# Kernel tuning notes

Measured on AMD Instinct MI355X. Metric: run time of the kernel, lower is better.

## Reference

```python
import jax, jax.numpy as jnp
import numpy as np

D = 256    # lstm_encoder_size
B = 1024   # batch (number of agents/trajectories)
T = 512    # prediction horizon (recurrence steps)
EPS = 1e-5


def setup_inputs() -> dict:
    key = jax.random.key(0)
    k = jax.random.split(key, 10)
    s = 1.0 / np.sqrt(D)
    return {
        "KS_ALL": jax.random.normal(k[0], (1, B, D), jnp.float32),
        "next_vf": jax.random.normal(k[1], (B, T), jnp.float32),
        # Koopman operators (torch Linear stores [out, in]; no bias)
        "A_w": jax.random.normal(k[2], (D, D), jnp.float32) * (0.4 * s),  # contractive
        "B_w": jax.random.normal(k[3], (D, 1), jnp.float32) * s,
        # decoder params (liner_dec=False)
        "W0": jax.random.normal(k[4], (2 * D, D), jnp.float32) * s,
        "b0": jnp.zeros((2 * D,), jnp.float32),
        "W1": jax.random.normal(k[5], (D, 2 * D), jnp.float32) / np.sqrt(2.0 * D),
        "b1": jnp.zeros((D,), jnp.float32),
        "ln_g": jnp.ones((D,), jnp.float32),
        "ln_b": jnp.zeros((D,), jnp.float32),
        "W2": jax.random.normal(k[6], (D, D), jnp.float32) * s,
        "b2": jnp.zeros((D,), jnp.float32),
        "W3": jax.random.normal(k[7], (3, D), jnp.float32) * s,
        "b3": jnp.zeros((3,), jnp.float32),
    }


def _layer_norm(x, g, b):
    mu = jnp.mean(x, axis=-1, keepdims=True)
    var = jnp.var(x, axis=-1, keepdims=True)
    return (x - mu) * jax.lax.rsqrt(var + EPS) * g + b


def reference(KS_ALL, next_vf, A_w, B_w, W0, b0, W1, b1, ln_g, ln_b, W2, b2, W3, b3):
    # train_flag=True -> use only the first time slice of KS_ALL
    ks0 = KS_ALL[0]                 # [B, D]
    u = next_vf.T                   # [T, B] time-major, matches permute(1,0,2)
    b_vec = B_w[:, 0]               # [D]  (Linear(1, D) on scalar input)

    def step(ks, u_t):
        ks_new = ks @ A_w.T + u_t[:, None] * b_vec[None, :]  # [B, D]
        return ks_new, ks_new

    _, ks_seq = jax.lax.scan(step, ks0, u)                   # [T, B, D]
    KS_pre = jnp.concatenate([ks0[None], ks_seq], axis=0)    # [T+1, B, D]

    # nonlinear decoder (eval mode: dropout is identity; use_elu=True)
    s1 = jnp.tanh(KS_pre @ W0.T + b0)          # [T+1, B, 2D]
    s2 = jnp.tanh(s1 @ W1.T + b1)              # [T+1, B, D]
    s2 = _layer_norm(KS_pre + s2, ln_g, ln_b)  # AddAndNorm
    s3 = jax.nn.elu(s2 @ W2.T + b2)
    OS = s3 @ W3.T + b3                        # [T+1, B, 3]
    return KS_pre, OS
```

## Files before the change

### kernel.cpp

```cpp
#include <hip/hip_runtime.h>

typedef unsigned short u16;
typedef __attribute__((ext_vector_type(8))) short bf16x8;
typedef __attribute__((ext_vector_type(4))) short bf16x4;
typedef __attribute__((ext_vector_type(4))) float f32x4;

#define MFMA16(a, b, c) __builtin_amdgcn_mfma_f32_16x16x32_bf16((a), (b), (c), 0, 0, 0)

#define OFF_UPAD 0
#define OFF_KS0  589824
#define OFF_W0   851968
#define OFF_W1   983040
#define OFF_W2   1114112
#define OFF_CRT  1179648
#define OFF_P    1196032
#define OFF_H1   5455872
#define OFF_S2   73089024
#define WS_END_U16 106905600ULL
#define OS_OFF   134479872

__device__ __forceinline__ u16 f2bf(float f) {
  union { float f; unsigned int i; } v; v.f = f;
  return (u16)((v.i + 0x7fffu + ((v.i >> 16) & 1u)) >> 16);
}
__device__ __forceinline__ float bf2f(u16 u) {
  union { unsigned int i; float f; } v; v.i = ((unsigned int)u) << 16;
  return v.f;
}
__device__ __forceinline__ float fast_tanh(float x) {
  float e = __expf(2.0f * x);
  return 1.0f - __fdividef(2.0f, e + 1.0f);
}

__global__ void k_prep(const float* __restrict__ KS_ALL, const float* __restrict__ next_vf,
                       const float* __restrict__ A_w, const float* __restrict__ W0,
                       const float* __restrict__ W1, const float* __restrict__ W2,
                       u16* __restrict__ ws) {
  int idx = blockIdx.x * 256 + threadIdx.x;
  if (idx < 589824) {
    int r = idx / 576, c = idx % 576;
    ws[OFF_UPAD + idx] = (c < 64) ? (u16)0 : f2bf(next_vf[r * 512 + c - 64]);
    return;
  }
  idx -= 589824;
  if (idx < 262144) { ws[OFF_KS0 + idx] = f2bf(KS_ALL[idx]); return; }
  idx -= 262144;
  if (idx < 131072) { ws[OFF_W0 + idx] = f2bf(W0[idx]); return; }
  idx -= 131072;
  if (idx < 131072) { ws[OFF_W1 + idx] = f2bf(W1[idx]); return; }
  idx -= 131072;
  if (idx < 65536)  { ws[OFF_W2 + idx] = f2bf(W2[idx]); return; }
  idx -= 65536;
  if (idx < 65536) {
    int r = idx >> 8, c = idx & 255;
    ws[OFF_P + idx] = (r == c) ? (u16)0x3F80 : (u16)0;
    ws[OFF_P + 65536 + idx] = f2bf(A_w[idx]);
  }
}

__global__ __launch_bounds__(512) void k_pow(u16* __restrict__ ws, int s) {
  const u16* P = ws + OFF_P;
  int j = blockIdx.y + 1;
  int mh = blockIdx.x;
  int lane = threadIdx.x & 63, w = threadIdx.x >> 6;
  int wm = w >> 2, wn = w & 3;
  int lg = lane >> 4, ll = lane & 15;
  const u16* Am = P + s * 65536;
  const u16* Bm = P + j * 65536;
  f32x4 acc[4][4];
  f32x4 z = {0.f, 0.f, 0.f, 0.f};
#pragma unroll
  for (int mi = 0; mi < 4; ++mi)
#pragma unroll
    for (int ni = 0; ni < 4; ++ni) acc[mi][ni] = z;
#pragma unroll
  for (int ks = 0; ks < 8; ++ks) {
    bf16x8 a[4], b[4];
    int kk = ks * 32 + lg * 8;
#pragma unroll
    for (int mi = 0; mi < 4; ++mi) {
      int row = mh * 128 + wm * 64 + mi * 16 + ll;
      a[mi] = *(const bf16x8*)(Am + row * 256 + kk);
    }
#pragma unroll
    for (int ni = 0; ni < 4; ++ni) {
      int col = wn * 64 + ni * 16 + ll;
#pragma unroll
      for (int e = 0; e < 8; ++e) b[ni][e] = (short)Bm[(kk + e) * 256 + col];
    }
#pragma unroll
    for (int mi = 0; mi < 4; ++mi)
#pragma unroll
      for (int ni = 0; ni < 4; ++ni) acc[mi][ni] = MFMA16(a[mi], b[ni], acc[mi][ni]);
  }
  u16* Pd = ws + OFF_P + (s + j) * 65536;
#pragma unroll
  for (int mi = 0; mi < 4; ++mi)
#pragma unroll
    for (int ni = 0; ni < 4; ++ni)
#pragma unroll
      for (int r = 0; r < 4; ++r) {
        int row = mh * 128 + wm * 64 + mi * 16 + lg * 4 + r;
        int col = wn * 64 + ni * 16 + ll;
        Pd[row * 256 + col] = f2bf(acc[mi][ni][r]);
      }
}

__global__ void k_crevt(const float* __restrict__ B_w, u16* __restrict__ ws) {
  int s = blockIdx.x;
  int n = threadIdx.x;
  const u16* Pr = ws + OFF_P + (63 - s) * 65536 + n * 256;
  float acc = 0.f;
  for (int k = 0; k < 256; ++k) acc += bf2f(Pr[k]) * B_w[k];
  ws[OFF_CRT + n * 64 + s] = f2bf(acc);
}


__global__ __launch_bounds__(512) void k_ks(const u16* __restrict__ ws, float* __restrict__ out) {
  __shared__ __align__(16) float Hf[32 * 260];
  const int t  = blockIdx.y;
  const int R0 = blockIdx.x * 64;
  const int tid = threadIdx.x;
  const int lane = tid & 63, w = tid >> 6;
  const int lg = lane >> 4, ll = lane & 15;
  f32x4 z = {0.f, 0.f, 0.f, 0.f};

  f32x4 acc[4][2];
#pragma unroll
  for (int mi = 0; mi < 4; ++mi)
#pragma unroll
    for (int ni = 0; ni < 2; ++ni) acc[mi][ni] = z;
  {
    const u16* CrevT = ws + OFF_CRT;
#pragma unroll
    for (int ksu = 0; ksu < 2; ++ksu) {
      bf16x8 au[4];
#pragma unroll
      for (int mi = 0; mi < 4; ++mi) {
        const u16* up = ws + OFF_UPAD + (R0 + mi * 16 + ll) * 576 + t + ksu * 32 + lg * 8;
#pragma unroll
        for (int e = 0; e < 8; ++e) au[mi][e] = (short)up[e];
      }
#pragma unroll
      for (int ni = 0; ni < 2; ++ni) {
        int n = w * 32 + ni * 16 + ll;
        bf16x8 bfr = *(const bf16x8*)(CrevT + n * 64 + ksu * 32 + lg * 8);
#pragma unroll
        for (int mi = 0; mi < 4; ++mi) acc[mi][ni] = MFMA16(au[mi], bfr, acc[mi][ni]);
      }
    }
    if (t < 64) {
      const u16* Pt = ws + OFF_P + t * 65536;
      const u16* ks0b = ws + OFF_KS0;
#pragma unroll
      for (int ks = 0; ks < 8; ++ks) {
        bf16x8 a[4], b[2];
#pragma unroll
        for (int mi = 0; mi < 4; ++mi)
          a[mi] = *(const bf16x8*)(ks0b + (R0 + mi * 16 + ll) * 256 + ks * 32 + lg * 8);
#pragma unroll
        for (int ni = 0; ni < 2; ++ni)
          b[ni] = *(const bf16x8*)(Pt + (w * 32 + ni * 16 + ll) * 256 + ks * 32 + lg * 8);
#pragma unroll
        for (int mi = 0; mi < 4; ++mi)
#pragma unroll
          for (int ni = 0; ni < 2; ++ni) acc[mi][ni] = MFMA16(a[mi], b[ni], acc[mi][ni]);
      }
    }
  }
#pragma unroll 1
  for (int p = 0; p < 2; ++p) {
#pragma unroll
    for (int mi2 = 0; mi2 < 2; ++mi2) {
      int mi = p * 2 + mi2;
#pragma unroll
      for (int ni = 0; ni < 2; ++ni)
#pragma unroll
        for (int r = 0; r < 4; ++r)
          Hf[(mi2 * 16 + lg * 4 + r) * 260 + w * 32 + ni * 16 + ll] = acc[mi][ni][r];
    }
    __syncthreads();
    float* ob = out + (size_t)t * 262144 + (size_t)(R0 + p * 32) * 256;
#pragma unroll
    for (int it = 0; it < 4; ++it) {
      int idx = it * 512 + tid;
      int row = idx >> 6, c4 = idx & 63;
      f32x4 v = *(const f32x4*)(Hf + row * 260 + c4 * 4);
      *(f32x4*)(ob + row * 256 + c4 * 4) = v;
    }
    __syncthreads();
  }
}

__global__ __launch_bounds__(512) void k_l1(const u16* __restrict__ ws,
                                            const float* __restrict__ outf,
                                            const float* __restrict__ b0,
                                            u16* __restrict__ h1, int t0) {
  __shared__ __align__(16) u16 Xb[16896];
  __shared__ __align__(16) u16 Hb[16896];
  __shared__ float pb0s[512];
  const int by = blockIdx.y;
  const int t  = t0 + by;
  const int R0 = blockIdx.x * 64;
  const int tid = threadIdx.x;
  const int lane = tid & 63, w = tid >> 6;
  const int lg = lane >> 4, ll = lane & 15;
  f32x4 z = {0.f, 0.f, 0.f, 0.f};

  pb0s[tid] = b0[tid];
  {
    const float* xs = outf + (size_t)t * 262144 + (size_t)R0 * 256;
#pragma unroll
    for (int it = 0; it < 8; ++it) {
      int idx = it * 512 + tid;
      int row = idx >> 6, c4 = idx & 63;
      f32x4 v = *(const f32x4*)(xs + row * 256 + c4 * 4);
      bf16x4 h;
#pragma unroll
      for (int e = 0; e < 4; ++e) h[e] = (short)f2bf(v[e]);
      int byt = (((row << 9) + ((c4 >> 1) << 4)) ^ ((row & 7) << 4)) + ((c4 & 1) << 3);
      *(bf16x4*)(Xb + (byt >> 1)) = h;
    }
  }
  __syncthreads();

  const u16* W0b = ws + OFF_W0;
#pragma unroll 1
  for (int nh = 0; nh < 2; ++nh) {
    f32x4 acc[4][2];
#pragma unroll
    for (int mi = 0; mi < 4; ++mi)
#pragma unroll
      for (int ni = 0; ni < 2; ++ni) acc[mi][ni] = z;
#pragma unroll
    for (int ks = 0; ks < 8; ++ks) {
      bf16x8 b[2];
#pragma unroll
      for (int ni = 0; ni < 2; ++ni) {
        int n = nh * 256 + w * 32 + ni * 16 + ll;
        b[ni] = *(const bf16x8*)(W0b + n * 256 + ks * 32 + lg * 8);
      }
#pragma unroll
      for (int mi = 0; mi < 4; ++mi) {
        int rl = mi * 16 + ll;
        int byt = ((rl << 9) + ks * 64 + (lg << 4)) ^ ((rl & 7) << 4);
        bf16x8 a = *(const bf16x8*)(Xb + (byt >> 1));
#pragma unroll
        for (int ni = 0; ni < 2; ++ni) acc[mi][ni] = MFMA16(a, b[ni], acc[mi][ni]);
      }
    }
#pragma unroll
    for (int mi = 0; mi < 4; ++mi)
#pragma unroll
      for (int ni = 0; ni < 2; ++ni)
#pragma unroll
        for (int r = 0; r < 4; ++r) {
          int rl = mi * 16 + lg * 4 + r;
          int col = w * 32 + ni * 16 + ll;
          Hb[rl * 264 + col] = f2bf(fast_tanh(acc[mi][ni][r] + pb0s[nh * 256 + col]));
        }
    __syncthreads();
    u16* hd = h1 + ((size_t)(by * 1024 + R0)) * 512 + nh * 256;
#pragma unroll
    for (int it = 0; it < 4; ++it) {
      int idx = it * 512 + tid;
      int row = idx >> 5, cq = idx & 31;
      bf16x8 v = *(const bf16x8*)(Hb + row * 264 + cq * 8);
      *(bf16x8*)(hd + row * 512 + cq * 8) = v;
    }
    __syncthreads();
  }
}

__global__ __launch_bounds__(512) void k_l2(const u16* __restrict__ ws,
                                            const float* __restrict__ outf,
                                            const float* __restrict__ b1,
                                            const float* __restrict__ lng,
                                            const float* __restrict__ lnb,
                                            const u16* __restrict__ h1,
                                            u16* __restrict__ s2, int t0) {
  __shared__ __align__(16) u16 Hs[16896];
  __shared__ __align__(16) u16 Rb[16896];
  __shared__ float par[768];
  float* pb1 = par;
  float* pg  = par + 256;
  float* pbt = par + 512;
  const int by = blockIdx.y;
  const int t  = t0 + by;
  const int R0 = blockIdx.x * 64;
  const int tid = threadIdx.x;
  const int lane = tid & 63, w = tid >> 6;
  const int lg = lane >> 4, ll = lane & 15;
  f32x4 z = {0.f, 0.f, 0.f, 0.f};

  if (tid < 256) { pb1[tid] = b1[tid]; pg[tid] = lng[tid]; pbt[tid] = lnb[tid]; }

  f32x4 accL2[4][2];
#pragma unroll
  for (int mi = 0; mi < 4; ++mi)
#pragma unroll
    for (int ni = 0; ni < 2; ++ni) accL2[mi][ni] = z;

  const u16* W1b = ws + OFF_W1;
  const u16* h1b = h1 + ((size_t)(by * 1024 + R0)) * 512;
#pragma unroll 1
  for (int kh = 0; kh < 2; ++kh) {
#pragma unroll
    for (int it = 0; it < 4; ++it) {
      int idx = it * 512 + tid;
      int row = idx >> 5, cq = idx & 31;
      bf16x8 v = *(const bf16x8*)(h1b + row * 512 + kh * 256 + cq * 8);
      int byt = ((row << 9) + (cq << 4)) ^ ((row & 7) << 4);
      *(bf16x8*)(Hs + (byt >> 1)) = v;
    }
    __syncthreads();
#pragma unroll
    for (int ks = 0; ks < 8; ++ks) {
      bf16x8 b[2];
#pragma unroll
      for (int ni = 0; ni < 2; ++ni) {
        int n = w * 32 + ni * 16 + ll;
        b[ni] = *(const bf16x8*)(W1b + n * 512 + kh * 256 + ks * 32 + lg * 8);
      }
#pragma unroll
      for (int mi = 0; mi < 4; ++mi) {
        int rl = mi * 16 + ll;
        int byt = ((rl << 9) + ks * 64 + (lg << 4)) ^ ((rl & 7) << 4);
        bf16x8 a = *(const bf16x8*)(Hs + (byt >> 1));
#pragma unroll
        for (int ni = 0; ni < 2; ++ni) accL2[mi][ni] = MFMA16(a, b[ni], accL2[mi][ni]);
      }
    }
    __syncthreads();
  }

  {
    const float* xs = outf + (size_t)t * 262144 + (size_t)R0 * 256;
#pragma unroll
    for (int mi = 0; mi < 4; ++mi)
#pragma unroll
      for (int ni = 0; ni < 2; ++ni)
#pragma unroll
        for (int r = 0; r < 4; ++r) {
          int rl = mi * 16 + lg * 4 + r;
          int col = w * 32 + ni * 16 + ll;
          float v = xs[rl * 256 + col] + fast_tanh(accL2[mi][ni][r] + pb1[col]);
          Rb[rl * 264 + col] = f2bf(v);
        }
  }
  __syncthreads();

  {
    int row = tid >> 3, jq = tid & 7;
    u16* hr = Rb + row * 264 + jq * 32;
    bf16x8 chv[4];
#pragma unroll
    for (int q = 0; q < 4; ++q) chv[q] = *(const bf16x8*)(hr + q * 8);
    float s = 0.f, ss = 0.f;
#pragma unroll
    for (int q = 0; q < 4; ++q)
#pragma unroll
      for (int e = 0; e < 8; ++e) { float v = bf2f((u16)chv[q][e]); s += v; ss += v * v; }
    s += __shfl_xor(s, 1);  s += __shfl_xor(s, 2);  s += __shfl_xor(s, 4);
    ss += __shfl_xor(ss, 1); ss += __shfl_xor(ss, 2); ss += __shfl_xor(ss, 4);
    float mu = s * 0.00390625f;
    float var = ss * 0.00390625f - mu * mu;
    float rstd = rsqrtf(var + 1e-5f);
#pragma unroll
    for (int q = 0; q < 4; ++q) {
      bf16x8 o;
#pragma unroll
      for (int e = 0; e < 8; ++e) {
        int col = jq * 32 + q * 8 + e;
        float v = (bf2f((u16)chv[q][e]) - mu) * rstd * pg[col] + pbt[col];
        o[e] = (short)f2bf(v);
      }
      *(bf16x8*)(hr + q * 8) = o;
    }
  }
  __syncthreads();

  {
    u16* sd = s2 + ((size_t)(by * 1024 + R0)) * 256;
#pragma unroll
    for (int it = 0; it < 4; ++it) {
      int idx = it * 512 + tid;
      int row = idx >> 5, cq = idx & 31;
      bf16x8 v = *(const bf16x8*)(Rb + row * 264 + cq * 8);
      *(bf16x8*)(sd + row * 256 + cq * 8) = v;
    }
  }
}

__global__ __launch_bounds__(512) void k_l3(const u16* __restrict__ ws,
                                            const float* __restrict__ b2,
                                            const float* __restrict__ W3,
                                            const float* __restrict__ b3,
                                            const u16* __restrict__ s2,
                                            float* __restrict__ out, int t0) {
  __shared__ __align__(16) u16 Sb[16896];
  __shared__ __align__(16) u16 Eb[16896];
  __shared__ float par[1028];
  float* pb2 = par;
  float* pW3 = par + 256;
  float* pb3 = par + 1024;
  const int by = blockIdx.y;
  const int t  = t0 + by;
  const int R0 = blockIdx.x * 64;
  const int tid = threadIdx.x;
  const int lane = tid & 63, w = tid >> 6;
  const int lg = lane >> 4, ll = lane & 15;
  f32x4 z = {0.f, 0.f, 0.f, 0.f};

  if (tid < 256) pb2[tid] = b2[tid];
  if (tid < 512) pW3[tid] = W3[tid];
  if (tid < 256) pW3[512 + tid] = W3[512 + tid];
  if (tid < 4) pb3[tid] = (tid < 3) ? b3[tid] : 0.f;

  {
    const u16* sb = s2 + ((size_t)(by * 1024 + R0)) * 256;
#pragma unroll
    for (int it = 0; it < 4; ++it) {
      int idx = it * 512 + tid;
      int row = idx >> 5, cq = idx & 31;
      bf16x8 v = *(const bf16x8*)(sb + row * 256 + cq * 8);
      int byt = ((row << 9) + (cq << 4)) ^ ((row & 7) << 4);
      *(bf16x8*)(Sb + (byt >> 1)) = v;
    }
  }
  __syncthreads();

  f32x4 acc[4][2];
#pragma unroll
  for (int mi = 0; mi < 4; ++mi)
#pragma unroll
    for (int ni = 0; ni < 2; ++ni) acc[mi][ni] = z;
  {
    const u16* W2b = ws + OFF_W2;
#pragma unroll
    for (int ks = 0; ks < 8; ++ks) {
      bf16x8 b[2];
#pragma unroll
      for (int ni = 0; ni < 2; ++ni) {
        int n = w * 32 + ni * 16 + ll;
        b[ni] = *(const bf16x8*)(W2b + n * 256 + ks * 32 + lg * 8);
      }
#pragma unroll
      for (int mi = 0; mi < 4; ++mi) {
        int rl = mi * 16 + ll;
        int byt = ((rl << 9) + ks * 64 + (lg << 4)) ^ ((rl & 7) << 4);
        bf16x8 a = *(const bf16x8*)(Sb + (byt >> 1));
#pragma unroll
        for (int ni = 0; ni < 2; ++ni) acc[mi][ni] = MFMA16(a, b[ni], acc[mi][ni]);
      }
    }
  }
#pragma unroll
  for (int mi = 0; mi < 4; ++mi)
#pragma unroll
    for (int ni = 0; ni < 2; ++ni)
#pragma unroll
      for (int r = 0; r < 4; ++r) {
        int rl = mi * 16 + lg * 4 + r;
        int col = w * 32 + ni * 16 + ll;
        float v = acc[mi][ni][r] + pb2[col];
        v = v > 0.f ? v : (__expf(v) - 1.f);
        Eb[rl * 264 + col] = f2bf(v);
      }
  __syncthreads();

  {
    int row = tid >> 3, jq = tid & 7;
    const u16* xr = Eb + row * 264 + jq * 32;
    float d0 = 0.f, d1 = 0.f, d2 = 0.f;
#pragma unroll
    for (int q = 0; q < 4; ++q) {
      bf16x8 c = *(const bf16x8*)(xr + q * 8);
#pragma unroll
      for (int e = 0; e < 8; ++e) {
        float v = bf2f((u16)c[e]);
        int col = jq * 32 + q * 8 + e;
        d0 += v * pW3[col]; d1 += v * pW3[256 + col]; d2 += v * pW3[512 + col];
      }
    }
    d0 += __shfl_xor(d0, 1); d0 += __shfl_xor(d0, 2); d0 += __shfl_xor(d0, 4);
    d1 += __shfl_xor(d1, 1); d1 += __shfl_xor(d1, 2); d1 += __shfl_xor(d1, 4);
    d2 += __shfl_xor(d2, 1); d2 += __shfl_xor(d2, 2); d2 += __shfl_xor(d2, 4);
    if (jq == 0) {
      int grow = R0 + row;
      int ob = OS_OFF + t * 3072 + grow * 3;
      out[ob]     = d0 + pb3[0];
      out[ob + 1] = d1 + pb3[1];
      out[ob + 2] = d2 + pb3[2];
    }
  }
}

__global__ __launch_bounds__(512) void k_fused(
    const u16* __restrict__ ws,
    const float* __restrict__ b0, const float* __restrict__ b1,
    const float* __restrict__ lng, const float* __restrict__ lnb,
    const float* __restrict__ b2, const float* __restrict__ W3,
    const float* __restrict__ b3, float* __restrict__ out) {
  __shared__ __align__(16) u16 Xb[16896];
  __shared__ __align__(16) unsigned char Hraw[33792];
  __shared__ float par[2308];
  u16* Hb = (u16*)Hraw;
  float* Hf = (float*)Hraw;
  float* pb0 = par;
  float* pb1 = par + 512;
  float* pg  = par + 768;
  float* pbt = par + 1024;
  float* pb2 = par + 1280;
  float* pW3 = par + 1536;
  float* pb3 = par + 2304;
  const int t  = blockIdx.y;
  const int R0 = blockIdx.x * 64;
  const int tid = threadIdx.x;
  const int lane = tid & 63, w = tid >> 6;
  const int lg = lane >> 4, ll = lane & 15;
  pb0[tid] = b0[tid];
  if (tid < 256) { pb1[tid] = b1[tid]; pg[tid] = lng[tid]; pbt[tid] = lnb[tid]; pb2[tid] = b2[tid]; }
  if (tid < 512) pW3[tid] = W3[tid];
  if (tid < 256) pW3[512 + tid] = W3[512 + tid];
  if (tid < 4) pb3[tid] = (tid < 3) ? b3[tid] : 0.f;
  f32x4 z = {0.f, 0.f, 0.f, 0.f};
  f32x4 acc[4][2];
#pragma unroll
  for (int mi = 0; mi < 4; ++mi)
#pragma unroll
    for (int ni = 0; ni < 2; ++ni) acc[mi][ni] = z;
  {
    const u16* CrevT = ws + OFF_CRT;
#pragma unroll
    for (int ksu = 0; ksu < 2; ++ksu) {
      bf16x8 au[4];
#pragma unroll
      for (int mi = 0; mi < 4; ++mi) {
        const u16* up = ws + OFF_UPAD + (R0 + mi * 16 + ll) * 576 + t + ksu * 32 + lg * 8;
#pragma unroll
        for (int e = 0; e < 8; ++e) au[mi][e] = (short)up[e];
      }
#pragma unroll
      for (int ni = 0; ni < 2; ++ni) {
        int n = w * 32 + ni * 16 + ll;
        bf16x8 bfr = *(const bf16x8*)(CrevT + n * 64 + ksu * 32 + lg * 8);
#pragma unroll
        for (int mi = 0; mi < 4; ++mi) acc[mi][ni] = MFMA16(au[mi], bfr, acc[mi][ni]);
      }
    }
    if (t < 64) {
      const u16* Pt = ws + OFF_P + t * 65536;
      const u16* ks0b = ws + OFF_KS0;
#pragma unroll
      for (int ks = 0; ks < 8; ++ks) {
        bf16x8 a[4], b[2];
#pragma unroll
        for (int mi = 0; mi < 4; ++mi)
          a[mi] = *(const bf16x8*)(ks0b + (R0 + mi * 16 + ll) * 256 + ks * 32 + lg * 8);
#pragma unroll
        for (int ni = 0; ni < 2; ++ni)
          b[ni] = *(const bf16x8*)(Pt + (w * 32 + ni * 16 + ll) * 256 + ks * 32 + lg * 8);
#pragma unroll
        for (int mi = 0; mi < 4; ++mi)
#pragma unroll
          for (int ni = 0; ni < 2; ++ni) acc[mi][ni] = MFMA16(a[mi], b[ni], acc[mi][ni]);
      }
    }
  }
#pragma unroll 1
  for (int p = 0; p < 2; ++p) {
#pragma unroll
    for (int mi2 = 0; mi2 < 2; ++mi2) {
      int mi = p * 2 + mi2;
#pragma unroll
      for (int ni = 0; ni < 2; ++ni)
#pragma unroll
        for (int r = 0; r < 4; ++r)
          Hf[(mi2 * 16 + lg * 4 + r) * 260 + w * 32 + ni * 16 + ll] = acc[mi][ni][r];
    }
    __syncthreads();
    float* ob = out + (size_t)t * 262144 + (size_t)(R0 + p * 32) * 256;
#pragma unroll
    for (int it = 0; it < 4; ++it) {
      int idx = it * 512 + tid;
      int row = idx >> 6, c4 = idx & 63;
      f32x4 v = *(const f32x4*)(Hf + row * 260 + c4 * 4);
      *(f32x4*)(ob + row * 256 + c4 * 4) = v;
      int rl = p * 32 + row;
      bf16x4 h;
#pragma unroll
      for (int e = 0; e < 4; ++e) h[e] = (short)f2bf(v[e]);
      int byt = (((rl << 9) + ((c4 >> 1) << 4)) ^ ((rl & 7) << 4)) + ((c4 & 1) << 3);
      *(bf16x4*)(Xb + (byt >> 1)) = h;
    }
    __syncthreads();
  }
  const u16* W0b = ws + OFF_W0;
  const u16* W1b = ws + OFF_W1;
  f32x4 accL2[4][2];
#pragma unroll
  for (int mi = 0; mi < 4; ++mi)
#pragma unroll
    for (int ni = 0; ni < 2; ++ni) accL2[mi][ni] = z;
  const int colL1 = w * 16 + ll;
#pragma unroll 1
  for (int q = 0; q < 4; ++q) {
    f32x4 accQ[4];
#pragma unroll
    for (int mi = 0; mi < 4; ++mi) accQ[mi] = z;
#pragma unroll
    for (int ks = 0; ks < 8; ++ks) {
      bf16x8 b = *(const bf16x8*)(W0b + (q * 128 + colL1) * 256 + ks * 32 + lg * 8);
#pragma unroll
      for (int mi = 0; mi < 4; ++mi) {
        int rl = mi * 16 + ll;
        int byt = ((rl << 9) + ks * 64 + (lg << 4)) ^ ((rl & 7) << 4);
        bf16x8 a = *(const bf16x8*)(Xb + (byt >> 1));
        accQ[mi] = MFMA16(a, b, accQ[mi]);
      }
    }
#pragma unroll
    for (int mi = 0; mi < 4; ++mi)
#pragma unroll
      for (int r = 0; r < 4; ++r) {
        int rl2 = mi * 16 + lg * 4 + r;
        float v = fast_tanh(accQ[mi][r] + pb0[q * 128 + colL1]);
        int byt = ((rl2 << 8) + (colL1 << 1)) ^ ((rl2 & 7) << 4);
        Hb[byt >> 1] = f2bf(v);
      }
    __syncthreads();
#pragma unroll
    for (int ks2 = 0; ks2 < 4; ++ks2) {
      bf16x8 bf0 = *(const bf16x8*)(W1b + (w * 32 + ll) * 512 + q * 128 + ks2 * 32 + lg * 8);
      bf16x8 bf1 = *(const bf16x8*)(W1b + (w * 32 + 16 + ll) * 512 + q * 128 + ks2 * 32 + lg * 8);
#pragma unroll
      for (int mi = 0; mi < 4; ++mi) {
        int rl = mi * 16 + ll;
        int byt = ((rl << 8) + ks2 * 64 + (lg << 4)) ^ ((rl & 7) << 4);
        bf16x8 a = *(const bf16x8*)(Hb + (byt >> 1));
        accL2[mi][0] = MFMA16(a, bf0, accL2[mi][0]);
        accL2[mi][1] = MFMA16(a, bf1, accL2[mi][1]);
      }
    }
    __syncthreads();
  }
#pragma unroll
  for (int mi = 0; mi < 4; ++mi)
#pragma unroll
    for (int ni = 0; ni < 2; ++ni)
#pragma unroll
      for (int r = 0; r < 4; ++r) {
        int rl = mi * 16 + lg * 4 + r;
        int col = w * 32 + ni * 16 + ll;
        float v = fast_tanh(accL2[mi][ni][r] + pb1[col]);
        int bx = ((rl << 9) + (col << 1)) ^ ((rl & 7) << 4);
        v += bf2f(Xb[bx >> 1]);
        Hb[rl * 264 + col] = f2bf(v);
      }
  __syncthreads();
  {
    int row = tid >> 3, jq = tid & 7;
    u16* hr = Hb + row * 264 + jq * 32;
    bf16x8 chv[4];
#pragma unroll
    for (int q = 0; q < 4; ++q) chv[q] = *(const bf16x8*)(hr + q * 8);
    float s = 0.f, ss = 0.f;
#pragma unroll
    for (int q = 0; q < 4; ++q)
#pragma unroll
      for (int e = 0; e < 8; ++e) { float v = bf2f((u16)chv[q][e]); s += v; ss += v * v; }
    s += __shfl_xor(s, 1);  s += __shfl_xor(s, 2);  s += __shfl_xor(s, 4);
    ss += __shfl_xor(ss, 1); ss += __shfl_xor(ss, 2); ss += __shfl_xor(ss, 4);
    float mu = s * 0.00390625f;
    float var = ss * 0.00390625f - mu * mu;
    float rstd = rsqrtf(var + 1e-5f);
#pragma unroll
    for (int q = 0; q < 4; ++q) {
      bf16x8 o;
#pragma unroll
      for (int e = 0; e < 8; ++e) {
        int col = jq * 32 + q * 8 + e;
        float v = (bf2f((u16)chv[q][e]) - mu) * rstd * pg[col] + pbt[col];
        o[e] = (short)f2bf(v);
      }
      *(bf16x8*)(hr + q * 8) = o;
    }
  }
  __syncthreads();
  {
    const u16* W2b = ws + OFF_W2;
    f32x4 a3[4][2];
#pragma unroll
    for (int mi = 0; mi < 4; ++mi)
#pragma unroll
      for (int ni = 0; ni < 2; ++ni) a3[mi][ni] = z;
#pragma unroll
    for (int ks = 0; ks < 8; ++ks) {
      bf16x8 bf0 = *(const bf16x8*)(W2b + (w * 32 + ll) * 256 + ks * 32 + lg * 8);
      bf16x8 bf1 = *(const bf16x8*)(W2b + (w * 32 + 16 + ll) * 256 + ks * 32 + lg * 8);
#pragma unroll
      for (int mi = 0; mi < 4; ++mi) {
        int rl = mi * 16 + ll;
        bf16x8 a = *(const bf16x8*)(Hb + rl * 264 + ks * 32 + lg * 8);
        a3[mi][0] = MFMA16(a, bf0, a3[mi][0]);
        a3[mi][1] = MFMA16(a, bf1, a3[mi][1]);
      }
    }
#pragma unroll
    for (int mi = 0; mi < 4; ++mi)
#pragma unroll
      for (int ni = 0; ni < 2; ++ni)
#pragma unroll
        for (int r = 0; r < 4; ++r) {
          int rl = mi * 16 + lg * 4 + r;
          int col = w * 32 + ni * 16 + ll;
          float v = a3[mi][ni][r] + pb2[col];
          v = v > 0.f ? v : (__expf(v) - 1.f);
          Xb[rl * 264 + col] = f2bf(v);
        }
  }
  __syncthreads();
  {
    int row = tid >> 3, jq = tid & 7;
    const u16* xr = Xb + row * 264 + jq * 32;
    float d0 = 0.f, d1 = 0.f, d2 = 0.f;
#pragma unroll
    for (int q = 0; q < 4; ++q) {
      bf16x8 c = *(const bf16x8*)(xr + q * 8);
#pragma unroll
      for (int e = 0; e < 8; ++e) {
        float v = bf2f((u16)c[e]);
        int col = jq * 32 + q * 8 + e;
        d0 += v * pW3[col]; d1 += v * pW3[256 + col]; d2 += v * pW3[512 + col];
      }
    }
    d0 += __shfl_xor(d0, 1); d0 += __shfl_xor(d0, 2); d0 += __shfl_xor(d0, 4);
    d1 += __shfl_xor(d1, 1); d1 += __shfl_xor(d1, 2); d1 += __shfl_xor(d1, 4);
    d2 += __shfl_xor(d2, 1); d2 += __shfl_xor(d2, 2); d2 += __shfl_xor(d2, 4);
    if (jq == 0) {
      int grow = R0 + row;
      int ob = OS_OFF + t * 3072 + grow * 3;
      out[ob]     = d0 + pb3[0];
      out[ob + 1] = d1 + pb3[1];
      out[ob + 2] = d2 + pb3[2];
    }
  }
}

extern "C" void kernel_launch(void* const* d_in, const int* in_sizes, int n_in,
                              void* d_out, int out_size, void* d_ws, size_t ws_size,
                              hipStream_t stream) {
  const float* KS_ALL  = (const float*)d_in[0];
  const float* next_vf = (const float*)d_in[1];
  const float* A_w     = (const float*)d_in[2];
  const float* B_w     = (const float*)d_in[3];
  const float* W0      = (const float*)d_in[4];
  const float* b0      = (const float*)d_in[5];
  const float* W1      = (const float*)d_in[6];
  const float* b1      = (const float*)d_in[7];
  const float* lng     = (const float*)d_in[8];
  const float* lnb     = (const float*)d_in[9];
  const float* W2      = (const float*)d_in[10];
  const float* b2      = (const float*)d_in[11];
  const float* W3      = (const float*)d_in[12];
  const float* b3      = (const float*)d_in[13];
  u16* ws = (u16*)d_ws;
  float* out = (float*)d_out;

  k_prep<<<4864, 256, 0, stream>>>(KS_ALL, next_vf, A_w, W0, W1, W2, ws);
  for (int s = 1; s <= 32; s <<= 1)
    k_pow<<<dim3(2, s), 512, 0, stream>>>(ws, s);
  k_crevt<<<64, 256, 0, stream>>>(B_w, ws);

  if (ws_size >= WS_END_U16 * 2ULL) {
    k_ks<<<dim3(16, 513), 512, 0, stream>>>(ws, out);
    u16* h1 = ws + OFF_H1;
    u16* s2 = ws + OFF_S2;
    const int t0s[4] = {0, 129, 257, 385};
    const int nts[4] = {129, 128, 128, 128};
    for (int c = 0; c < 4; ++c) {
      k_l1<<<dim3(16, nts[c]), 512, 0, stream>>>(ws, out, b0, h1, t0s[c]);
      k_l2<<<dim3(16, nts[c]), 512, 0, stream>>>(ws, out, b1, lng, lnb, h1, s2, t0s[c]);
      k_l3<<<dim3(16, nts[c]), 512, 0, stream>>>(ws, b2, W3, b3, s2, out, t0s[c]);
    }
  } else {
    k_fused<<<dim3(16, 513), 512, 0, stream>>>(ws, b0, b1, lng, lnb, b2, W3, b3, out);
  }
}
```

Measured before the change: 1.613 ms.

## Fuse decoder layers 2 and 3, pre-shift u into aligned copies, use nontemporal memory ops

Merges the layer-norm stage and the W2/ELU/W3 stage into one kernel, keeping the normalized activations in shared memory instead of writing and re-reading an s2 buffer. It also builds eight pre-shifted, zero-padded copies of the input sequence so the recurrence kernels can load the u operand with aligned 16-byte vector loads instead of scalar gathers. Large streaming reads and writes (KS output, h1, OS) now use nontemporal hints, and the OS results are staged in shared memory for coalesced vector stores. The cost is a larger prep kernel that writes about eight times more u data, and more shared memory per block in the fused kernel, which may lower occupancy.

```diff
diff --git a/kernel.cpp b/kernel.cpp
--- a/kernel.cpp
+++ b/kernel.cpp
@@ -7,16 +7,16 @@
 
 #define MFMA16(a, b, c) __builtin_amdgcn_mfma_f32_16x16x32_bf16((a), (b), (c), 0, 0, 0)
 
-#define OFF_UPAD 0
-#define OFF_KS0  589824
-#define OFF_W0   851968
-#define OFF_W1   983040
-#define OFF_W2   1114112
-#define OFF_CRT  1179648
-#define OFF_P    1196032
-#define OFF_H1   5455872
-#define OFF_S2   73089024
-#define WS_END_U16 106905600ULL
+#define OFF_U8   0
+#define U8_CPY   598016
+#define OFF_KS0  4784128
+#define OFF_W0   5046272
+#define OFF_W1   5177344
+#define OFF_W2   5308416
+#define OFF_CRT  5373952
+#define OFF_P    5390336
+#define OFF_H1   9650176
+#define WS_END_U16 77283328ULL
 #define OS_OFF   134479872
 
 __device__ __forceinline__ u16 f2bf(float f) {
@@ -37,12 +37,16 @@
                        const float* __restrict__ W1, const float* __restrict__ W2,
                        u16* __restrict__ ws) {
   int idx = blockIdx.x * 256 + threadIdx.x;
-  if (idx < 589824) {
-    int r = idx / 576, c = idx % 576;
-    ws[OFF_UPAD + idx] = (c < 64) ? (u16)0 : f2bf(next_vf[r * 512 + c - 64]);
+  if (idx < 4784128) {
+    int p = idx / U8_CPY;
+    int rem = idx - p * U8_CPY;
+    int b = rem / 584;
+    int c = rem - b * 584;
+    int col = c + p;
+    ws[OFF_U8 + idx] = (col >= 64 && col < 576) ? f2bf(next_vf[b * 512 + col - 64]) : (u16)0;
     return;
   }
-  idx -= 589824;
+  idx -= 4784128;
   if (idx < 262144) { ws[OFF_KS0 + idx] = f2bf(KS_ALL[idx]); return; }
   idx -= 262144;
   if (idx < 131072) { ws[OFF_W0 + idx] = f2bf(W0[idx]); return; }
@@ -132,15 +136,13 @@
     for (int ni = 0; ni < 2; ++ni) acc[mi][ni] = z;
   {
     const u16* CrevT = ws + OFF_CRT;
+    const u16* u8b = ws + OFF_U8 + (size_t)(t & 7) * U8_CPY + (t & ~7);
 #pragma unroll
     for (int ksu = 0; ksu < 2; ++ksu) {
       bf16x8 au[4];
 #pragma unroll
-      for (int mi = 0; mi < 4; ++mi) {
-        const u16* up = ws + OFF_UPAD + (R0 + mi * 16 + ll) * 576 + t + ksu * 32 + lg * 8;
-#pragma unroll
-        for (int e = 0; e < 8; ++e) au[mi][e] = (short)up[e];
-      }
+      for (int mi = 0; mi < 4; ++mi)
+        au[mi] = *(const bf16x8*)(u8b + (R0 + mi * 16 + ll) * 584 + ksu * 32 + lg * 8);
 #pragma unroll
       for (int ni = 0; ni < 2; ++ni) {
         int n = w * 32 + ni * 16 + ll;
@@ -186,7 +188,7 @@
       int idx = it * 512 + tid;
       int row = idx >> 6, c4 = idx & 63;
       f32x4 v = *(const f32x4*)(Hf + row * 260 + c4 * 4);
-      *(f32x4*)(ob + row * 256 + c4 * 4) = v;
+      __builtin_nontemporal_store(v, (f32x4*)(ob + row * 256 + c4 * 4));
     }
     __syncthreads();
   }
@@ -214,7 +216,7 @@
     for (int it = 0; it < 8; ++it) {
       int idx = it * 512 + tid;
       int row = idx >> 6, c4 = idx & 63;
-      f32x4 v = *(const f32x4*)(xs + row * 256 + c4 * 4);
+      f32x4 v = __builtin_nontemporal_load((const f32x4*)(xs + row * 256 + c4 * 4));
       bf16x4 h;
 #pragma unroll
       for (int e = 0; e < 4; ++e) h[e] = (short)f2bf(v[e]);
@@ -266,25 +268,32 @@
       int idx = it * 512 + tid;
       int row = idx >> 5, cq = idx & 31;
       bf16x8 v = *(const bf16x8*)(Hb + row * 264 + cq * 8);
-      *(bf16x8*)(hd + row * 512 + cq * 8) = v;
-    }
-    __syncthreads();
-  }
-}
-
-__global__ __launch_bounds__(512) void k_l2(const u16* __restrict__ ws,
-                                            const float* __restrict__ outf,
-                                            const float* __restrict__ b1,
-                                            const float* __restrict__ lng,
-                                            const float* __restrict__ lnb,
-                                            const u16* __restrict__ h1,
-                                            u16* __restrict__ s2, int t0) {
+      __builtin_nontemporal_store(v, (bf16x8*)(hd + row * 512 + cq * 8));
+    }
+    __syncthreads();
+  }
+}
+
+__global__ __launch_bounds__(512) void k_l23(const u16* __restrict__ ws,
+                                             const float* __restrict__ outf,
+                                             const float* __restrict__ b1,
+                                             const float* __restrict__ lng,
+                                             const float* __restrict__ lnb,
+                                             const float* __restrict__ b2,
+                                             const float* __restrict__ W3,
+                                             const float* __restrict__ b3,
+                                             const u16* __restrict__ h1,
+                                             float* __restrict__ out, int t0) {
   __shared__ __align__(16) u16 Hs[16896];
   __shared__ __align__(16) u16 Rb[16896];
-  __shared__ float par[768];
+  __shared__ float par[1796];
+  __shared__ float osb[208];
   float* pb1 = par;
   float* pg  = par + 256;
   float* pbt = par + 512;
+  float* pb2 = par + 768;
+  float* pW3 = par + 1024;
+  float* pb3 = par + 1792;
   const int by = blockIdx.y;
   const int t  = t0 + by;
   const int R0 = blockIdx.x * 64;
@@ -293,7 +302,10 @@
   const int lg = lane >> 4, ll = lane & 15;
   f32x4 z = {0.f, 0.f, 0.f, 0.f};
 
-  if (tid < 256) { pb1[tid] = b1[tid]; pg[tid] = lng[tid]; pbt[tid] = lnb[tid]; }
+  if (tid < 256) { pb1[tid] = b1[tid]; pg[tid] = lng[tid]; pbt[tid] = lnb[tid]; pb2[tid] = b2[tid]; }
+  if (tid < 512) pW3[tid] = W3[tid];
+  if (tid < 256) pW3[512 + tid] = W3[512 + tid];
+  if (tid < 4) pb3[tid] = (tid < 3) ? b3[tid] : 0.f;
 
   f32x4 accL2[4][2];
 #pragma unroll
@@ -309,7 +321,7 @@
     for (int it = 0; it < 4; ++it) {
       int idx = it * 512 + tid;
       int row = idx >> 5, cq = idx & 31;
-      bf16x8 v = *(const bf16x8*)(h1b + row * 512 + kh * 256 + cq * 8);
+      bf16x8 v = __builtin_nontemporal_load((const bf16x8*)(h1b + row * 512 + kh * 256 + cq * 8));
       int byt = ((row << 9) + (cq << 4)) ^ ((row & 7) << 4);
       *(bf16x8*)(Hs + (byt >> 1)) = v;
     }
@@ -344,7 +356,8 @@
         for (int r = 0; r < 4; ++r) {
           int rl = mi * 16 + lg * 4 + r;
           int col = w * 32 + ni * 16 + ll;
-          float v = xs[rl * 256 + col] + fast_tanh(accL2[mi][ni][r] + pb1[col]);
+          float xv = __builtin_nontemporal_load(xs + rl * 256 + col);
+          float v = xv + fast_tanh(accL2[mi][ni][r] + pb1[col]);
           Rb[rl * 264 + col] = f2bf(v);
         }
   }
@@ -381,62 +394,12 @@
   __syncthreads();
 
   {
-    u16* sd = s2 + ((size_t)(by * 1024 + R0)) * 256;
-#pragma unroll
-    for (int it = 0; it < 4; ++it) {
-      int idx = it * 512 + tid;
-      int row = idx >> 5, cq = idx & 31;
-      bf16x8 v = *(const bf16x8*)(Rb + row * 264 + cq * 8);
-      *(bf16x8*)(sd + row * 256 + cq * 8) = v;
-    }
-  }
-}
-
-__global__ __launch_bounds__(512) void k_l3(const u16* __restrict__ ws,
-                                            const float* __restrict__ b2,
-                                            const float* __restrict__ W3,
-                                            const float* __restrict__ b3,
-                                            const u16* __restrict__ s2,
-                                            float* __restrict__ out, int t0) {
-  __shared__ __align__(16) u16 Sb[16896];
-  __shared__ __align__(16) u16 Eb[16896];
-  __shared__ float par[1028];
-  float* pb2 = par;
-  float* pW3 = par + 256;
-  float* pb3 = par + 1024;
-  const int by = blockIdx.y;
-  const int t  = t0 + by;
-  const int R0 = blockIdx.x * 64;
-  const int tid = threadIdx.x;
-  const int lane = tid & 63, w = tid >> 6;
-  const int lg = lane >> 4, ll = lane & 15;
-  f32x4 z = {0.f, 0.f, 0.f, 0.f};
-
-  if (tid < 256) pb2[tid] = b2[tid];
-  if (tid < 512) pW3[tid] = W3[tid];
-  if (tid < 256) pW3[512 + tid] = W3[512 + tid];
-  if (tid < 4) pb3[tid] = (tid < 3) ? b3[tid] : 0.f;
-
-  {
-    const u16* sb = s2 + ((size_t)(by * 1024 + R0)) * 256;
-#pragma unroll
-    for (int it = 0; it < 4; ++it) {
-      int idx = it * 512 + tid;
-      int row = idx >> 5, cq = idx & 31;
-      bf16x8 v = *(const bf16x8*)(sb + row * 256 + cq * 8);
-      int byt = ((row << 9) + (cq << 4)) ^ ((row & 7) << 4);
-      *(bf16x8*)(Sb + (byt >> 1)) = v;
-    }
-  }
-  __syncthreads();
-
-  f32x4 acc[4][2];
-#pragma unroll
-  for (int mi = 0; mi < 4; ++mi)
-#pragma unroll
-    for (int ni = 0; ni < 2; ++ni) acc[mi][ni] = z;
-  {
     const u16* W2b = ws + OFF_W2;
+    f32x4 a3[4][2];
+#pragma unroll
+    for (int mi = 0; mi < 4; ++mi)
+#pragma unroll
+      for (int ni = 0; ni < 2; ++ni) a3[mi][ni] = z;
 #pragma unroll
     for (int ks = 0; ks < 8; ++ks) {
       bf16x8 b[2];
@@ -448,30 +411,29 @@
 #pragma unroll
       for (int mi = 0; mi < 4; ++mi) {
         int rl = mi * 16 + ll;
-        int byt = ((rl << 9) + ks * 64 + (lg << 4)) ^ ((rl & 7) << 4);
-        bf16x8 a = *(const bf16x8*)(Sb + (byt >> 1));
-#pragma unroll
-        for (int ni = 0; ni < 2; ++ni) acc[mi][ni] = MFMA16(a, b[ni], acc[mi][ni]);
-      }
-    }
-  }
-#pragma unroll
-  for (int mi = 0; mi < 4; ++mi)
-#pragma unroll
-    for (int ni = 0; ni < 2; ++ni)
-#pragma unroll
-      for (int r = 0; r < 4; ++r) {
-        int rl = mi * 16 + lg * 4 + r;
-        int col = w * 32 + ni * 16 + ll;
-        float v = acc[mi][ni][r] + pb2[col];
-        v = v > 0.f ? v : (__expf(v) - 1.f);
-        Eb[rl * 264 + col] = f2bf(v);
-      }
+        bf16x8 a = *(const bf16x8*)(Rb + rl * 264 + ks * 32 + lg * 8);
+#pragma unroll
+        for (int ni = 0; ni < 2; ++ni) a3[mi][ni] = MFMA16(a, b[ni], a3[mi][ni]);
+      }
+    }
+#pragma unroll
+    for (int mi = 0; mi < 4; ++mi)
+#pragma unroll
+      for (int ni = 0; ni < 2; ++ni)
+#pragma unroll
+        for (int r = 0; r < 4; ++r) {
+          int rl = mi * 16 + lg * 4 + r;
+          int col = w * 32 + ni * 16 + ll;
+          float v = a3[mi][ni][r] + pb2[col];
+          v = v > 0.f ? v : (__expf(v) - 1.f);
+          Hs[rl * 264 + col] = f2bf(v);
+        }
+  }
   __syncthreads();
 
   {
     int row = tid >> 3, jq = tid & 7;
-    const u16* xr = Eb + row * 264 + jq * 32;
+    const u16* xr = Hs + row * 264 + jq * 32;
     float d0 = 0.f, d1 = 0.f, d2 = 0.f;
 #pragma unroll
     for (int q = 0; q < 4; ++q) {
@@ -487,12 +449,15 @@
     d1 += __shfl_xor(d1, 1); d1 += __shfl_xor(d1, 2); d1 += __shfl_xor(d1, 4);
     d2 += __shfl_xor(d2, 1); d2 += __shfl_xor(d2, 2); d2 += __shfl_xor(d2, 4);
     if (jq == 0) {
-      int grow = R0 + row;
-      int ob = OS_OFF + t * 3072 + grow * 3;
-      out[ob]     = d0 + pb3[0];
-      out[ob + 1] = d1 + pb3[1];
-      out[ob + 2] = d2 + pb3[2];
-    }
+      osb[row * 3]     = d0 + pb3[0];
+      osb[row * 3 + 1] = d1 + pb3[1];
+      osb[row * 3 + 2] = d2 + pb3[2];
+    }
+  }
+  __syncthreads();
+  if (tid < 48) {
+    f32x4 v = *(const f32x4*)(osb + tid * 4);
+    __builtin_nontemporal_store(v, (f32x4*)(out + OS_OFF + (size_t)t * 3072 + (size_t)R0 * 3 + tid * 4));
   }
 }
 
@@ -532,15 +497,13 @@
     for (int ni = 0; ni < 2; ++ni) acc[mi][ni] = z;
   {
     const u16* CrevT = ws + OFF_CRT;
+    const u16* u8b = ws + OFF_U8 + (size_t)(t & 7) * U8_CPY + (t & ~7);
 #pragma unroll
     for (int ksu = 0; ksu < 2; ++ksu) {
       bf16x8 au[4];
 #pragma unroll
-      for (int mi = 0; mi < 4; ++mi) {
-        const u16* up = ws + OFF_UPAD + (R0 + mi * 16 + ll) * 576 + t + ksu * 32 + lg * 8;
-#pragma unroll
-        for (int e = 0; e < 8; ++e) au[mi][e] = (short)up[e];
-      }
+      for (int mi = 0; mi < 4; ++mi)
+        au[mi] = *(const bf16x8*)(u8b + (R0 + mi * 16 + ll) * 584 + ksu * 32 + lg * 8);
 #pragma unroll
       for (int ni = 0; ni < 2; ++ni) {
         int n = w * 32 + ni * 16 + ll;
@@ -768,7 +731,7 @@
   u16* ws = (u16*)d_ws;
   float* out = (float*)d_out;
 
-  k_prep<<<4864, 256, 0, stream>>>(KS_ALL, next_vf, A_w, W0, W1, W2, ws);
+  k_prep<<<21248, 256, 0, stream>>>(KS_ALL, next_vf, A_w, W0, W1, W2, ws);
   for (int s = 1; s <= 32; s <<= 1)
     k_pow<<<dim3(2, s), 512, 0, stream>>>(ws, s);
   k_crevt<<<64, 256, 0, stream>>>(B_w, ws);
@@ -776,13 +739,11 @@
   if (ws_size >= WS_END_U16 * 2ULL) {
     k_ks<<<dim3(16, 513), 512, 0, stream>>>(ws, out);
     u16* h1 = ws + OFF_H1;
-    u16* s2 = ws + OFF_S2;
     const int t0s[4] = {0, 129, 257, 385};
     const int nts[4] = {129, 128, 128, 128};
     for (int c = 0; c < 4; ++c) {
       k_l1<<<dim3(16, nts[c]), 512, 0, stream>>>(ws, out, b0, h1, t0s[c]);
-      k_l2<<<dim3(16, nts[c]), 512, 0, stream>>>(ws, out, b1, lng, lnb, h1, s2, t0s[c]);
-      k_l3<<<dim3(16, nts[c]), 512, 0, stream>>>(ws, b2, W3, b3, s2, out, t0s[c]);
+      k_l23<<<dim3(16, nts[c]), 512, 0, stream>>>(ws, out, b1, lng, lnb, b2, W3, b3, h1, out, t0s[c]);
     }
   } else {
     k_fused<<<dim3(16, 513), 512, 0, stream>>>(ws, b0, b1, lng, lnb, b2, W3, b3, out);
```

After: 1.377 ms. 14.7% less time.
